# Kernel tuning notes

Measured on AMD Instinct MI355X. Metric: run time of the kernel, lower is better.

## Reference

```python
import jax, jax.numpy as jnp
import numpy as np

DIM = 1024
HEADS = 16
DHEAD = 64
WIDTH = 512
INNER = HEADS * DHEAD  # 1024
BATCH = 2
SEQ = 4096  # divisible by WIDTH -> 8 blocks


def setup_inputs() -> dict:
    key = jax.random.key(0)
    ks = jax.random.split(key, 6)
    x = jax.random.normal(ks[0], (BATCH, SEQ, DIM), jnp.float32)
    # bias broadcast over (b, w) onto sim of shape [b, w, h, WIDTH, 2*WIDTH]
    rel_pos_bias = jax.random.normal(ks[1], (HEADS, WIDTH, 2 * WIDTH), jnp.float32)
    # stacked (past_k, past_v), each [b, h, WIDTH, d]
    xl_memories = jax.random.normal(ks[2], (2, BATCH, HEADS, WIDTH, DHEAD), jnp.float32)
    gamma = jnp.ones((DIM,), jnp.float32)
    w_qkv = jax.random.normal(ks[3], (DIM, 3 * INNER), jnp.float32) * 0.02
    w_out = jax.random.normal(ks[4], (INNER, DIM), jnp.float32) * 0.02
    return {"x": x, "rel_pos_bias": rel_pos_bias, "xl_memories": xl_memories,
            "gamma": gamma, "w_qkv": w_qkv, "w_out": w_out}


def reference(x, rel_pos_bias, xl_memories, gamma, w_qkv, w_out):
    b, seq, dim = x.shape
    w = seq // WIDTH
    # LayerNorm (beta buffer is zeros in the module)
    mu = jnp.mean(x, axis=-1, keepdims=True)
    var = jnp.var(x, axis=-1, keepdims=True)
    xn = (x - mu) * jax.lax.rsqrt(var + 1e-5) * gamma
    # qkv projection, split heads, blockify: [b, w, h, WIDTH, d]
    qkv = xn @ w_qkv
    q, k, v = jnp.split(qkv, 3, axis=-1)
    def to_blocks(t):
        return t.reshape(b, w, WIDTH, HEADS, DHEAD).transpose(0, 1, 3, 2, 4)
    bq, bk, bv = map(to_blocks, (q, k, v))
    # new XL memories: last block's k/v -> [2, b, h, WIDTH, d]
    memories = jnp.stack((bk[:, -1], bv[:, -1]))
    # prepend past block of k/v
    past_k = xl_memories[0][:, None]  # [b, 1, h, WIDTH, d]
    past_v = xl_memories[1][:, None]
    bk = jnp.concatenate((past_k, bk), axis=1)  # [b, w+1, h, WIDTH, d]
    bv = jnp.concatenate((past_v, bv), axis=1)
    # sliding 2-block kv window: [b, w, h, 2*WIDTH, d]
    bk = jnp.concatenate((bk[:, :-1], bk[:, 1:]), axis=-2)
    bv = jnp.concatenate((bv[:, :-1], bv[:, 1:]), axis=-2)
    # attention with rel-pos bias and causal mask (i=WIDTH queries, j=2*WIDTH keys)
    scale = DHEAD ** -0.5
    sim = jnp.einsum('bwhid,bwhjd->bwhij', bq, bk) * scale + rel_pos_bias
    i, j = WIDTH, 2 * WIDTH
    causal_mask = jnp.triu(jnp.ones((i, j), bool), j - i + 1)
    neg = -jnp.finfo(sim.dtype).max
    sim = jnp.where(causal_mask, neg, sim)
    attn = jax.nn.softmax(sim, axis=-1)
    out = jnp.einsum('bwhij,bwhjd->bwhid', attn, bv)
    # merge blocks and heads back: [b, seq, inner]
    out = out.transpose(0, 1, 3, 2, 4).reshape(b, seq, INNER)
    out = out[:, :seq]
    return out @ w_out, memories
```

## Files before the change

### kernel.cpp

```cpp
#include <hip/hip_runtime.h>
#include <hip/hip_bf16.h>

#define DIMV   1024
#define HEADSV 16
#define DHEADV 64
#define WIDTHV 512
#define INNERV 1024
#define BATCHV 2
#define SEQV   4096
#define NROWS  (BATCHV*SEQV)
#define KVROWS (WIDTHV + SEQV)

#define LOG2E 1.4426950408889634f

typedef short bf16x8 __attribute__((ext_vector_type(8)));
typedef short bf16x4 __attribute__((ext_vector_type(4)));
typedef int   int4v  __attribute__((ext_vector_type(4)));
typedef float f32x4  __attribute__((ext_vector_type(4)));

typedef const __attribute__((address_space(1))) void* gvp;
typedef __attribute__((address_space(3))) void* lvp;

static __device__ __forceinline__ short f2bf(float f) {
  __hip_bfloat16 h = __float2bfloat16(f);
  return __builtin_bit_cast(short, h);
}
static __device__ __forceinline__ float bf2f(short s) {
  unsigned u = ((unsigned)(unsigned short)s) << 16;
  return __builtin_bit_cast(float, u);
}
static __device__ __forceinline__ bf16x8 ntload8(const short* p) {
  int4v v = __builtin_nontemporal_load((const int4v*)p);
  return __builtin_bit_cast(bf16x8, v);
}

__global__ __launch_bounds__(256) void ln_kernel(const float* __restrict__ x,
                                                 const float* __restrict__ gamma,
                                                 short* __restrict__ xn) {
  int row = blockIdx.x;
  int t = threadIdx.x;
  const float* xr = x + (size_t)row * DIMV;
  float4 v = reinterpret_cast<const float4*>(xr)[t];
  float s  = v.x + v.y + v.z + v.w;
  float sq = v.x*v.x + v.y*v.y + v.z*v.z + v.w*v.w;
  #pragma unroll
  for (int o = 32; o > 0; o >>= 1) { s += __shfl_down(s, o); sq += __shfl_down(sq, o); }
  __shared__ float red[8];
  int wv = t >> 6;
  if ((t & 63) == 0) { red[wv] = s; red[4 + wv] = sq; }
  __syncthreads();
  s  = red[0] + red[1] + red[2] + red[3];
  sq = red[4] + red[5] + red[6] + red[7];
  float mean = s * (1.0f/1024.0f);
  float var  = sq * (1.0f/1024.0f) - mean*mean;
  float rstd = rsqrtf(var + 1e-5f);
  float4 g = reinterpret_cast<const float4*>(gamma)[t];
  short4 o4;
  o4.x = f2bf((v.x - mean) * rstd * g.x);
  o4.y = f2bf((v.y - mean) * rstd * g.y);
  o4.z = f2bf((v.z - mean) * rstd * g.z);
  o4.w = f2bf((v.w - mean) * rstd * g.w);
  reinterpret_cast<short4*>(xn + (size_t)row * DIMV)[t] = o4;
}

__global__ __launch_bounds__(256) void transpose_f32_bf16(const float* __restrict__ in,
                                                          short* __restrict__ out,
                                                          int R, int C) {
  __shared__ float tile[32][33];
  int tc = blockIdx.x * 32;
  int tr = blockIdx.y * 32;
  int tx = threadIdx.x & 31, ty = threadIdx.x >> 5;
  #pragma unroll
  for (int i = 0; i < 32; i += 8)
    tile[ty + i][tx] = in[(size_t)(tr + ty + i) * C + tc + tx];
  __syncthreads();
  #pragma unroll
  for (int i = 0; i < 32; i += 8)
    out[(size_t)(tc + ty + i) * R + tr + tx] = f2bf(tile[tx][ty + i]);
}

__global__ __launch_bounds__(256) void pack_bias(const float* __restrict__ in,
                                                 short* __restrict__ out) {
  int idx = blockIdx.x * 256 + threadIdx.x;
  int j   = idx & 1023;
  int ir4 = (idx >> 10) & 127;
  int h   = idx >> 17;
  const float* src = in + ((size_t)(h*512 + ir4*4))*1024 + j;
  short4 o;
  o.x = f2bf(src[0]    * LOG2E);
  o.y = f2bf(src[1024] * LOG2E);
  o.z = f2bf(src[2048] * LOG2E);
  o.w = f2bf(src[3072] * LOG2E);
  *reinterpret_cast<short4*>(out + (size_t)idx*4) = o;
}

__global__ void xl_to_kv(const float* __restrict__ xl,
                         short* __restrict__ k_all, short* __restrict__ v_all) {
  int tid = blockIdx.x * 256 + threadIdx.x;
  int d = (tid & 15) * 4;
  int rest = tid >> 4;
  int s = rest & 511; rest >>= 9;
  int h = rest & 15;  rest >>= 4;
  int b = rest & 1;   int m2 = rest >> 1;
  float4 v = *reinterpret_cast<const float4*>(
      xl + ((((size_t)((m2*2 + b)*16 + h))*512 + s)*64 + d));
  short4 o; o.x = f2bf(v.x); o.y = f2bf(v.y); o.z = f2bf(v.z); o.w = f2bf(v.w);
  short* dst = (m2 ? v_all : k_all) + (((size_t)(b*16 + h)*KVROWS + s)*64 + d);
  *reinterpret_cast<short4*>(dst) = o;
}

__global__ __launch_bounds__(256) void transpose_v(const short* __restrict__ v,
                                                   short* __restrict__ vt) {
  __shared__ __align__(16) short tile[64][72];
  int bh = blockIdx.y;
  int s0 = blockIdx.x * 64;
  int tid = threadIdx.x;
  const short* src = v + (size_t)bh * KVROWS * 64;
  #pragma unroll
  for (int p = 0; p < 2; ++p) {
    int flat = p*256 + tid;
    int row = flat >> 3, ch = flat & 7;
    int pch = ch ^ (row >> 3);
    *reinterpret_cast<int4v*>(&tile[row][pch*8]) =
      *reinterpret_cast<const int4v*>(src + (size_t)(s0 + row)*64 + ch*8);
  }
  __syncthreads();
  short* dst = vt + (size_t)bh * 64 * KVROWS;
  #pragma unroll
  for (int p = 0; p < 2; ++p) {
    int flat = p*256 + tid;
    int d = flat >> 3, sch = flat & 7;
    short tmp[8];
    #pragma unroll
    for (int k = 0; k < 8; ++k) {
      int s = sch*8 + k;
      int pch = (d >> 3) ^ (s >> 3);
      tmp[k] = tile[s][pch*8 + (d & 7)];
    }
    *reinterpret_cast<int4v*>(dst + (size_t)d*KVROWS + s0 + sch*8) =
      *reinterpret_cast<const int4v*>(tmp);
  }
}

template<int MODE>
__global__ __launch_bounds__(256) void gemm_bt(
    const short* __restrict__ A, const short* __restrict__ Bm,
    short* __restrict__ qo, short* __restrict__ ko, short* __restrict__ vo,
    float* __restrict__ memo, float* __restrict__ co, int N) {
  __shared__ __align__(16) short As[2][128*64];
  __shared__ __align__(16) short Bs[2][128*64];
  const int K = 1024;
  int bm = blockIdx.x * 128;
  int bn = blockIdx.y * 128;
  int tid = threadIdx.x;
  int lane = tid & 63, wid = tid >> 6;
  int wr = wid >> 1, wc = wid & 1;
  int fr = lane & 15, fq = lane >> 4;

  const int r0 = tid >> 3;
  const int sl = tid & 7;
  const int sc = sl ^ (r0 & 7);
  const short* agp = A  + (size_t)(bm + r0)*K + sc*8;
  const short* bgp = Bm + (size_t)(bn + r0)*K + sc*8;
  const int wbase = wid*64*8;

  f32x4 acc[4][4] = {};

  auto stage = [&](int bufi, int k0) {
    #pragma unroll
    for (int p = 0; p < 4; ++p) {
      __builtin_amdgcn_global_load_lds(
          (gvp)(const void*)(agp + (size_t)p*32*K + k0),
          (lvp)(void*)(&As[bufi][p*2048 + wbase]), 16, 0, 0);
      __builtin_amdgcn_global_load_lds(
          (gvp)(const void*)(bgp + (size_t)p*32*K + k0),
          (lvp)(void*)(&Bs[bufi][p*2048 + wbase]), 16, 0, 0);
    }
  };

  stage(0, 0);
  __syncthreads();

  for (int it = 0; it < 16; ++it) {
    const int buf = it & 1;
    if (it < 15) stage(buf ^ 1, (it + 1) * 64);
    __builtin_amdgcn_sched_barrier(0);
    #pragma unroll
    for (int kc = 0; kc < 2; ++kc) {
      const int ca = kc*4 + fq;
      bf16x8 af[4], bfr[4];
      #pragma unroll
      for (int i = 0; i < 4; ++i) {
        int ra = wr*64 + i*16 + fr;
        int rb = wc*64 + i*16 + fr;
        af[i]  = *reinterpret_cast<const bf16x8*>(&As[buf][ra*64 + (ca ^ (ra & 7))*8]);
        bfr[i] = *reinterpret_cast<const bf16x8*>(&Bs[buf][rb*64 + (ca ^ (rb & 7))*8]);
      }
      #pragma unroll
      for (int i = 0; i < 4; ++i)
        #pragma unroll
        for (int j = 0; j < 4; ++j)
          acc[i][j] = __builtin_amdgcn_mfma_f32_16x16x32_bf16(af[i], bfr[j], acc[i][j], 0, 0, 0);
    }
    __syncthreads();
  }

  if (MODE == 0) {
    #pragma unroll
    for (int i = 0; i < 4; ++i)
      #pragma unroll
      for (int j = 0; j < 4; ++j)
        #pragma unroll
        for (int r = 0; r < 4; ++r) {
          int m = bm + wr*64 + i*16 + fq*4 + r;
          int n = bn + wc*64 + j*16 + fr;
          float val = acc[i][j][r];
          int b = m >> 12, s = m & 4095;
          if (n < 1024) {
            qo[(size_t)m*1024 + n] = f2bf(val * (0.125f * LOG2E));
          } else {
            int h = (n >> 6) & 15, d = n & 63;
            size_t idx = ((size_t)((b << 4) + h)*KVROWS + 512 + s)*64 + d;
            if (n < 2048) ko[idx] = f2bf(val);
            else          vo[idx] = f2bf(val);
            if (s >= 3584) {
              int m2 = (n < 2048) ? 0 : 1;
              memo[((size_t)(((m2*2 + b) << 4) + h)*512 + (s - 3584))*64 + d] = val;
            }
          }
        }
  } else {
    #pragma unroll
    for (int i = 0; i < 4; ++i)
      #pragma unroll
      for (int j = 0; j < 4; ++j)
        #pragma unroll
        for (int r = 0; r < 4; ++r) {
          int m = bm + wr*64 + i*16 + fq*4 + r;
          int n = bn + wc*64 + j*16 + fr;
          co[(size_t)m*N + n] = acc[i][j][r];
        }
  }
}

__global__ __launch_bounds__(256, 2) void attn_kernel(
    const short* __restrict__ q,
    const short* __restrict__ k_all,
    const short* __restrict__ vt,
    const short* __restrict__ bp,
    short* __restrict__ attnb) {
  __shared__ __align__(16) short Ks[2][64*72];
  __shared__ __align__(16) short Pb[4][16*72];

  const int bid = blockIdx.x;
  const int h = bid & 15, w = (bid >> 4) & 7, b = (bid >> 7) & 1;
  const int cq = 3 - (bid >> 8);
  const int tid = threadIdx.x, lane = tid & 63, wid = tid >> 6;
  const int fr = lane & 15, fq = lane >> 4;
  const int qoff = cq*128 + wid*32;

  const short* qrow = q + ((size_t)(b*SEQV + w*WIDTHV + qoff))*1024 + h*64;
  bf16x8 qf[2][2];
  #pragma unroll
  for (int i = 0; i < 2; ++i)
    #pragma unroll
    for (int c = 0; c < 2; ++c)
      qf[i][c] = ntload8(qrow + (size_t)(i*16 + fr)*1024 + c*32 + fq*8);

  f32x4 o[2][4] = {};
  float racc[2][4] = {{0.f,0.f,0.f,0.f},{0.f,0.f,0.f,0.f}};

  const short* kg  = k_all + ((size_t)(b*16 + h)*KVROWS + w*512)*64;
  const short* vg  = vt    + (size_t)(b*16 + h)*64*KVROWS + w*512;
  const short* bpw = bp    + ((size_t)(h*128 + (qoff >> 2) + fq))*4096;

  const int sr = tid >> 3, sc = tid & 7;
  const short* kgs = kg + (size_t)sr*64 + sc*8;
  const int soA = sr*72 + sc*8;

  {
    int4v k0v[2];
    #pragma unroll
    for (int p = 0; p < 2; ++p)
      k0v[p] = *reinterpret_cast<const int4v*>(kgs + p*32*64);
    #pragma unroll
    for (int p = 0; p < 2; ++p)
      *reinterpret_cast<int4v*>(&Ks[0][soA + p*2304]) = k0v[p];
  }
  __syncthreads();

  const int NT = 2*cq + 10;
  const int tmaxw = 2*cq + 8 + (wid >> 1);

  for (int t = 0; t < NT; ++t) {
    const int buf = t & 1;
    int4v kk[2];
    const bool more = (t + 1 < NT);
    if (more) {
      #pragma unroll
      for (int p = 0; p < 2; ++p)
        kk[p] = *reinterpret_cast<const int4v*>(kgs + (size_t)(t+1)*4096 + p*32*64);
    }
    if (t <= tmaxw) {
      const int j0 = t * 64;
      bf16x4 bb[2][4];
      #pragma unroll
      for (int i = 0; i < 2; ++i)
        #pragma unroll
        for (int jc = 0; jc < 4; ++jc)
          bb[i][jc] = *reinterpret_cast<const bf16x4*>(
              &bpw[(size_t)i*16384 + (size_t)(j0 + jc*16 + fr)*4]);
      bf16x8 kf0[4], kf1[4];
      #pragma unroll
      for (int jc = 0; jc < 4; ++jc) {
        kf0[jc] = *reinterpret_cast<const bf16x8*>(&Ks[buf][(jc*16 + fr)*72 + fq*8]);
        kf1[jc] = *reinterpret_cast<const bf16x8*>(&Ks[buf][(jc*16 + fr)*72 + 32 + fq*8]);
      }
      bf16x8 vf[2][4];
      #pragma unroll
      for (int jk = 0; jk < 2; ++jk)
        #pragma unroll
        for (int dc = 0; dc < 4; ++dc)
          vf[jk][dc] = *reinterpret_cast<const bf16x8*>(
              vg + (size_t)(dc*16 + fr)*KVROWS + j0 + jk*32 + fq*8);

      f32x4 s[2][4];
      __builtin_amdgcn_s_setprio(1);
      #pragma unroll
      for (int i = 0; i < 2; ++i)
        #pragma unroll
        for (int jc = 0; jc < 4; ++jc) {
          f32x4 c;
          c[0] = bf2f(bb[i][jc][0]); c[1] = bf2f(bb[i][jc][1]);
          c[2] = bf2f(bb[i][jc][2]); c[3] = bf2f(bb[i][jc][3]);
          s[i][jc] = __builtin_amdgcn_mfma_f32_16x16x32_bf16(qf[i][0], kf0[jc], c, 0, 0, 0);
        }
      #pragma unroll
      for (int i = 0; i < 2; ++i)
        #pragma unroll
        for (int jc = 0; jc < 4; ++jc)
          s[i][jc] = __builtin_amdgcn_mfma_f32_16x16x32_bf16(qf[i][1], kf1[jc], s[i][jc], 0, 0, 0);
      __builtin_amdgcn_s_setprio(0);

      if (t == tmaxw) {
        #pragma unroll
        for (int i = 0; i < 2; ++i)
          #pragma unroll
          for (int jc = 0; jc < 4; ++jc)
            #pragma unroll
            for (int r = 0; r < 4; ++r)
              if (j0 + jc*16 + fr > qoff + i*16 + fq*4 + r + 512)
                s[i][jc][r] = -1e30f;
      }

      #pragma unroll
      for (int i = 0; i < 2; ++i) {
        short* Pw = &Pb[wid][0];
        #pragma unroll
        for (int jc = 0; jc < 4; ++jc)
          #pragma unroll
          for (int r = 0; r < 4; ++r) {
            float p = exp2f(fminf(s[i][jc][r], 80.f));
            racc[i][r] += p;
            Pw[(fq*4 + r)*72 + jc*16 + fr] = f2bf(p);
          }
        asm volatile("s_waitcnt lgkmcnt(0)" ::: "memory");
        __builtin_amdgcn_sched_barrier(0);
        __builtin_amdgcn_s_setprio(1);
        #pragma unroll
        for (int jk = 0; jk < 2; ++jk) {
          bf16x8 pf = *reinterpret_cast<const bf16x8*>(&Pw[fr*72 + jk*32 + fq*8]);
          #pragma unroll
          for (int dc = 0; dc < 4; ++dc)
            o[i][dc] = __builtin_amdgcn_mfma_f32_16x16x32_bf16(pf, vf[jk][dc], o[i][dc], 0, 0, 0);
        }
        __builtin_amdgcn_s_setprio(0);
        __builtin_amdgcn_sched_barrier(0);
      }
    }
    if (more) {
      #pragma unroll
      for (int p = 0; p < 2; ++p)
        *reinterpret_cast<int4v*>(&Ks[buf ^ 1][soA + p*2304]) = kk[p];
    }
    __syncthreads();
  }

  #pragma unroll
  for (int i = 0; i < 2; ++i)
    #pragma unroll
    for (int off = 1; off < 16; off <<= 1)
      #pragma unroll
      for (int r = 0; r < 4; ++r)
        racc[i][r] += __shfl_xor(racc[i][r], off);

  short* obase = attnb + ((size_t)(b*SEQV + w*WIDTHV + qoff))*1024 + h*64;
  #pragma unroll
  for (int i = 0; i < 2; ++i) {
    float inv[4];
    #pragma unroll
    for (int r = 0; r < 4; ++r) inv[r] = 1.0f / racc[i][r];
    #pragma unroll
    for (int dc = 0; dc < 4; ++dc)
      #pragma unroll
      for (int r = 0; r < 4; ++r)
        obase[(size_t)(i*16 + fq*4 + r)*1024 + dc*16 + fr] = f2bf(o[i][dc][r] * inv[r]);
  }
}

extern "C" void kernel_launch(void* const* d_in, const int* in_sizes, int n_in,
                              void* d_out, int out_size, void* d_ws, size_t ws_size,
                              hipStream_t stream) {
  const float* x     = (const float*)d_in[0];
  const float* bias  = (const float*)d_in[1];
  const float* xl    = (const float*)d_in[2];
  const float* gamma = (const float*)d_in[3];
  const float* w_qkv = (const float*)d_in[4];
  const float* w_out = (const float*)d_in[5];
  float* out = (float*)d_out;
  float* mem_out = out + (size_t)BATCHV*SEQV*DIMV;

  char* ws = (char*)d_ws;
  size_t off = 0;
  auto alloc = [&](size_t bytes) { size_t o = off; off += (bytes + 255) & ~(size_t)255; return o; };
  short* xn    = (short*)(ws + alloc((size_t)NROWS*DIMV*2));
  short* wqkvT = (short*)(ws + alloc((size_t)3*INNERV*DIMV*2));
  short* woutT = (short*)(ws + alloc((size_t)DIMV*INNERV*2));
  short* bp    = (short*)(ws + alloc((size_t)HEADSV*128*1024*4*2));
  short* qbuf  = (short*)(ws + alloc((size_t)NROWS*INNERV*2));
  short* k_all = (short*)(ws + alloc((size_t)BATCHV*HEADSV*KVROWS*DHEADV*2));
  short* v_all = (short*)(ws + alloc((size_t)BATCHV*HEADSV*KVROWS*DHEADV*2));
  short* vt    = (short*)(ws + alloc((size_t)BATCHV*HEADSV*KVROWS*DHEADV*2));
  short* attnb = xn;

  transpose_f32_bf16<<<dim3(3*INNERV/32, DIMV/32), 256, 0, stream>>>(w_qkv, wqkvT, DIMV, 3*INNERV);
  transpose_f32_bf16<<<dim3(INNERV/32, DIMV/32), 256, 0, stream>>>(w_out, woutT, DIMV, INNERV);
  pack_bias<<<8192, 256, 0, stream>>>(bias, bp);
  xl_to_kv<<<2048, 256, 0, stream>>>(xl, k_all, v_all);
  ln_kernel<<<NROWS, 256, 0, stream>>>(x, gamma, xn);
  gemm_bt<0><<<dim3(NROWS/128, (3*INNERV)/128), 256, 0, stream>>>(
      xn, wqkvT, qbuf, k_all, v_all, mem_out, nullptr, 3*INNERV);
  transpose_v<<<dim3(KVROWS/64, BATCHV*HEADSV), 256, 0, stream>>>(v_all, vt);
  attn_kernel<<<4*BATCHV*8*HEADSV, 256, 0, stream>>>(qbuf, k_all, vt, bp, attnb);
  gemm_bt<1><<<dim3(NROWS/128, INNERV/128), 256, 0, stream>>>(
      attnb, woutT, nullptr, nullptr, nullptr, nullptr, out, INNERV);
}
```

Baseline: 205.8 us.

## Load K fragments directly from global memory instead of double-buffered LDS

Drops the shared-memory double buffer for K tiles in the attention kernel. Each wave now reads its K MFMA fragments straight from global memory, the same way V is already read. This removes the per-iteration __syncthreads and the LDS staging traffic, and lets each wave stop at its own causal limit instead of running the block-wide tile count. In exchange the four waves in a block each load the same K rows from global memory, relying on L1/L2 for reuse. Without prefetch, more load latency is exposed.

New measurement: 241.2 us. +17.2%, slower.

```diff
diff --git a/kernel.cpp b/kernel.cpp
--- a/kernel.cpp
+++ b/kernel.cpp
@@ -249,7 +249,6 @@
     const short* __restrict__ vt,
     const short* __restrict__ bp,
     short* __restrict__ attnb) {
-  __shared__ __align__(16) short Ks[2][64*72];
   __shared__ __align__(16) short Pb[4][16*72];
 
   const int bid = blockIdx.x;
@@ -274,116 +273,86 @@
   const short* vg  = vt    + (size_t)(b*16 + h)*64*KVROWS + w*512;
   const short* bpw = bp    + ((size_t)(h*128 + (qoff >> 2) + fq))*4096;
 
-  const int sr = tid >> 3, sc = tid & 7;
-  const short* kgs = kg + (size_t)sr*64 + sc*8;
-  const int soA = sr*72 + sc*8;
-
-  {
-    int4v k0v[2];
-    #pragma unroll
-    for (int p = 0; p < 2; ++p)
-      k0v[p] = *reinterpret_cast<const int4v*>(kgs + p*32*64);
-    #pragma unroll
-    for (int p = 0; p < 2; ++p)
-      *reinterpret_cast<int4v*>(&Ks[0][soA + p*2304]) = k0v[p];
-  }
-  __syncthreads();
-
-  const int NT = 2*cq + 10;
   const int tmaxw = 2*cq + 8 + (wid >> 1);
 
-  for (int t = 0; t < NT; ++t) {
-    const int buf = t & 1;
-    int4v kk[2];
-    const bool more = (t + 1 < NT);
-    if (more) {
-      #pragma unroll
-      for (int p = 0; p < 2; ++p)
-        kk[p] = *reinterpret_cast<const int4v*>(kgs + (size_t)(t+1)*4096 + p*32*64);
-    }
-    if (t <= tmaxw) {
-      const int j0 = t * 64;
-      bf16x4 bb[2][4];
+  for (int t = 0; t <= tmaxw; ++t) {
+    const int j0 = t * 64;
+    bf16x8 kf0[4], kf1[4];
+    #pragma unroll
+    for (int jc = 0; jc < 4; ++jc) {
+      kf0[jc] = *reinterpret_cast<const bf16x8*>(
+          kg + (size_t)(j0 + jc*16 + fr)*64 + fq*8);
+      kf1[jc] = *reinterpret_cast<const bf16x8*>(
+          kg + (size_t)(j0 + jc*16 + fr)*64 + 32 + fq*8);
+    }
+    bf16x8 vf[2][4];
+    #pragma unroll
+    for (int jk = 0; jk < 2; ++jk)
+      #pragma unroll
+      for (int dc = 0; dc < 4; ++dc)
+        vf[jk][dc] = *reinterpret_cast<const bf16x8*>(
+            vg + (size_t)(dc*16 + fr)*KVROWS + j0 + jk*32 + fq*8);
+    bf16x4 bb[2][4];
+    #pragma unroll
+    for (int i = 0; i < 2; ++i)
+      #pragma unroll
+      for (int jc = 0; jc < 4; ++jc)
+        bb[i][jc] = *reinterpret_cast<const bf16x4*>(
+            &bpw[(size_t)i*16384 + (size_t)(j0 + jc*16 + fr)*4]);
+
+    f32x4 s[2][4];
+    __builtin_amdgcn_s_setprio(1);
+    #pragma unroll
+    for (int i = 0; i < 2; ++i)
+      #pragma unroll
+      for (int jc = 0; jc < 4; ++jc) {
+        f32x4 c;
+        c[0] = bf2f(bb[i][jc][0]); c[1] = bf2f(bb[i][jc][1]);
+        c[2] = bf2f(bb[i][jc][2]); c[3] = bf2f(bb[i][jc][3]);
+        s[i][jc] = __builtin_amdgcn_mfma_f32_16x16x32_bf16(qf[i][0], kf0[jc], c, 0, 0, 0);
+      }
+    #pragma unroll
+    for (int i = 0; i < 2; ++i)
+      #pragma unroll
+      for (int jc = 0; jc < 4; ++jc)
+        s[i][jc] = __builtin_amdgcn_mfma_f32_16x16x32_bf16(qf[i][1], kf1[jc], s[i][jc], 0, 0, 0);
+    __builtin_amdgcn_s_setprio(0);
+
+    if (t == tmaxw) {
       #pragma unroll
       for (int i = 0; i < 2; ++i)
-        #pragma unroll
-        for (int jc = 0; jc < 4; ++jc)
-          bb[i][jc] = *reinterpret_cast<const bf16x4*>(
-              &bpw[(size_t)i*16384 + (size_t)(j0 + jc*16 + fr)*4]);
-      bf16x8 kf0[4], kf1[4];
-      #pragma unroll
-      for (int jc = 0; jc < 4; ++jc) {
-        kf0[jc] = *reinterpret_cast<const bf16x8*>(&Ks[buf][(jc*16 + fr)*72 + fq*8]);
-        kf1[jc] = *reinterpret_cast<const bf16x8*>(&Ks[buf][(jc*16 + fr)*72 + 32 + fq*8]);
-      }
-      bf16x8 vf[2][4];
-      #pragma unroll
-      for (int jk = 0; jk < 2; ++jk)
-        #pragma unroll
-        for (int dc = 0; dc < 4; ++dc)
-          vf[jk][dc] = *reinterpret_cast<const bf16x8*>(
-              vg + (size_t)(dc*16 + fr)*KVROWS + j0 + jk*32 + fq*8);
-
-      f32x4 s[2][4];
-      __builtin_amdgcn_s_setprio(1);
-      #pragma unroll
-      for (int i = 0; i < 2; ++i)
-        #pragma unroll
-        for (int jc = 0; jc < 4; ++jc) {
-          f32x4 c;
-          c[0] = bf2f(bb[i][jc][0]); c[1] = bf2f(bb[i][jc][1]);
-          c[2] = bf2f(bb[i][jc][2]); c[3] = bf2f(bb[i][jc][3]);
-          s[i][jc] = __builtin_amdgcn_mfma_f32_16x16x32_bf16(qf[i][0], kf0[jc], c, 0, 0, 0);
-        }
-      #pragma unroll
-      for (int i = 0; i < 2; ++i)
-        #pragma unroll
-        for (int jc = 0; jc < 4; ++jc)
-          s[i][jc] = __builtin_amdgcn_mfma_f32_16x16x32_bf16(qf[i][1], kf1[jc], s[i][jc], 0, 0, 0);
-      __builtin_amdgcn_s_setprio(0);
-
-      if (t == tmaxw) {
-        #pragma unroll
-        for (int i = 0; i < 2; ++i)
-          #pragma unroll
-          for (int jc = 0; jc < 4; ++jc)
-            #pragma unroll
-            for (int r = 0; r < 4; ++r)
-              if (j0 + jc*16 + fr > qoff + i*16 + fq*4 + r + 512)
-                s[i][jc][r] = -1e30f;
-      }
-
-      #pragma unroll
-      for (int i = 0; i < 2; ++i) {
-        short* Pw = &Pb[wid][0];
         #pragma unroll
         for (int jc = 0; jc < 4; ++jc)
           #pragma unroll
-          for (int r = 0; r < 4; ++r) {
-            float p = exp2f(fminf(s[i][jc][r], 80.f));
-            racc[i][r] += p;
-            Pw[(fq*4 + r)*72 + jc*16 + fr] = f2bf(p);
-          }
-        asm volatile("s_waitcnt lgkmcnt(0)" ::: "memory");
-        __builtin_amdgcn_sched_barrier(0);
-        __builtin_amdgcn_s_setprio(1);
-        #pragma unroll
-        for (int jk = 0; jk < 2; ++jk) {
-          bf16x8 pf = *reinterpret_cast<const bf16x8*>(&Pw[fr*72 + jk*32 + fq*8]);
-          #pragma unroll
-          for (int dc = 0; dc < 4; ++dc)
-            o[i][dc] = __builtin_amdgcn_mfma_f32_16x16x32_bf16(pf, vf[jk][dc], o[i][dc], 0, 0, 0);
+          for (int r = 0; r < 4; ++r)
+            if (j0 + jc*16 + fr > qoff + i*16 + fq*4 + r + 512)
+              s[i][jc][r] = -1e30f;
+    }
+
+    #pragma unroll
+    for (int i = 0; i < 2; ++i) {
+      short* Pw = &Pb[wid][0];
+      #pragma unroll
+      for (int jc = 0; jc < 4; ++jc)
+        #pragma unroll
+        for (int r = 0; r < 4; ++r) {
+          float p = exp2f(fminf(s[i][jc][r], 80.f));
+          racc[i][r] += p;
+          Pw[(fq*4 + r)*72 + jc*16 + fr] = f2bf(p);
         }
-        __builtin_amdgcn_s_setprio(0);
-        __builtin_amdgcn_sched_barrier(0);
+      asm volatile("s_waitcnt lgkmcnt(0)" ::: "memory");
+      __builtin_amdgcn_sched_barrier(0);
+      __builtin_amdgcn_s_setprio(1);
+      #pragma unroll
+      for (int jk = 0; jk < 2; ++jk) {
+        bf16x8 pf = *reinterpret_cast<const bf16x8*>(&Pw[fr*72 + jk*32 + fq*8]);
+        #pragma unroll
+        for (int dc = 0; dc < 4; ++dc)
+          o[i][dc] = __builtin_amdgcn_mfma_f32_16x16x32_bf16(pf, vf[jk][dc], o[i][dc], 0, 0, 0);
       }
-    }
-    if (more) {
-      #pragma unroll
-      for (int p = 0; p < 2; ++p)
-        *reinterpret_cast<int4v*>(&Ks[buf ^ 1][soA + p*2304]) = kk[p];
-    }
-    __syncthreads();
+      __builtin_amdgcn_s_setprio(0);
+      __builtin_amdgcn_sched_barrier(0);
+    }
   }
 
   #pragma unroll
```
